# Optimization experiments

Measured on AMD Instinct MI355X. Metric: run time of the kernel, lower is better.

The kernel has to match this reference:

```python
import jax, jax.numpy as jnp
import numpy as np

DIM = 768
HEADS = 12
HD = DIM // HEADS  # 64
BASE = 100.0


def rope_sincos(H, W):
    # DINOv3 RopePositionEmbedding: normalize_coords='separate', base=100.0
    dd = HD // 4
    periods = BASE ** (jnp.arange(dd, dtype=jnp.float32) / dd)          # [dd]
    ch = (jnp.arange(H, dtype=jnp.float32) + 0.5) / H                    # pixel centers
    cw = (jnp.arange(W, dtype=jnp.float32) + 0.5) / W
    cy, cx = jnp.meshgrid(ch, cw, indexing='ij')
    coords = 2.0 * jnp.stack([cy, cx], axis=-1).reshape(H * W, 2) - 1.0  # [N,2] in [-1,1]
    angles = 2.0 * jnp.pi * coords[:, :, None] / periods[None, None, :]  # [N,2,dd]
    angles = angles.reshape(H * W, 2 * dd)                               # [N, HD//2]
    angles = jnp.concatenate([angles, angles], axis=-1)                  # [N, HD]
    return jnp.sin(angles), jnp.cos(angles)


def rotate_half(t):
    t1, t2 = jnp.split(t, 2, axis=-1)
    return jnp.concatenate([-t2, t1], axis=-1)


def setup_inputs() -> dict:
    key = jax.random.key(0)
    k1, k2, k3 = jax.random.split(key, 3)
    B, H, W = 2, 48, 48
    x = jax.random.normal(k1, (B, H, W, DIM), dtype=jnp.float32)
    w_qkv = jax.random.normal(k2, (3 * DIM, DIM), dtype=jnp.float32) * 0.02
    b_qkv = jnp.zeros((3 * DIM,), dtype=jnp.float32)
    w_proj = jax.random.normal(k3, (DIM, DIM), dtype=jnp.float32) * 0.02
    b_proj = jnp.zeros((DIM,), dtype=jnp.float32)
    return {"x": x, "w_qkv": w_qkv, "b_qkv": b_qkv, "w_proj": w_proj, "b_proj": b_proj}


def reference(x, w_qkv, b_qkv, w_proj, b_proj):
    B, H, W, C = x.shape
    N = H * W
    xf = x.reshape(B, N, C)
    qkv = xf @ w_qkv.T + b_qkv                                   # [B,N,3C]
    qkv = qkv.reshape(B, N, 3, HEADS, HD).transpose(2, 0, 3, 1, 4)
    q, k, v = qkv[0], qkv[1], qkv[2]                              # [B,h,N,d]
    sin, cos = rope_sincos(H, W)                                  # [N,d]
    q = q * cos + rotate_half(q) * sin
    k = k * cos + rotate_half(k) * sin
    scale = HD ** -0.5
    attn = jax.nn.softmax(jnp.einsum('bhqd,bhkd->bhqk', q, k) * scale, axis=-1)
    o = jnp.einsum('bhqk,bhkd->bhqd', attn, v)                    # [B,h,N,d]
    o = o.transpose(0, 2, 1, 3).reshape(B, N, C)
    o = o @ w_proj.T + b_proj
    return o.reshape(B, H, W, C)
```

## Files before the change

kernel.cpp:

```cpp
#include <hip/hip_runtime.h>

#define BATCH 2
#define NSEQ 2304
#define DIM 768
#define HEADS 12
#define HD 64
#define M_TOK (BATCH * NSEQ)
#define LDSP 72
#define KP 72
#define BH (BATCH * HEADS)
#define KT_HALF (NSEQ / 64 / 2)

typedef __attribute__((ext_vector_type(8))) short bf16x8;
typedef __attribute__((ext_vector_type(8))) short short8v;
typedef __attribute__((ext_vector_type(4))) float f32x4;
typedef __fp16 fp16x2 __attribute__((ext_vector_type(2)));
typedef _Float16 half4 __attribute__((ext_vector_type(4)));
typedef _Float16 half8 __attribute__((ext_vector_type(8)));

#define QSCALE (0.125f * 1.44269504088896f)
#define LOG2_100_D16 0.41524101186092029f

__device__ __forceinline__ short f2bf(float f) {
    union { float f; unsigned u; } v; v.f = f;
    unsigned r = v.u + 0x7fffu + ((v.u >> 16) & 1u);
    return (short)(r >> 16);
}

#define CN1 (M_TOK * DIM / 4)
#define CN2 (3 * DIM * DIM / 4)
#define CN3 (DIM * DIM / 4)
__global__ void cvt_all_kernel(const float* __restrict__ x, const float* __restrict__ wq,
                               const float* __restrict__ wp,
                               short* __restrict__ xb, short* __restrict__ wqb,
                               short* __restrict__ wpb) {
    int i = blockIdx.x * 256 + threadIdx.x;
    const float* src; short* dst; int j;
    if (i < CN1)              { src = x;  dst = xb;  j = i; }
    else if (i < CN1 + CN2)   { src = wq; dst = wqb; j = i - CN1; }
    else                      { src = wp; dst = wpb; j = i - CN1 - CN2; }
    float4 v = reinterpret_cast<const float4*>(src)[j];
    short4 o;
    o.x = f2bf(v.x); o.y = f2bf(v.y); o.z = f2bf(v.z); o.w = f2bf(v.w);
    reinterpret_cast<short4*>(dst)[j] = o;
}

__global__ __launch_bounds__(256) void gemm_qkv_kernel(
    const short* __restrict__ A,
    const short* __restrict__ Bt,
    const float* __restrict__ bias,
    short* __restrict__ qb, short* __restrict__ kbuf, _Float16* __restrict__ vtb)
{
    __shared__ __align__(16) short At[2][128 * LDSP];
    __shared__ __align__(16) short Bl[2][128 * LDSP];
    const int m0 = blockIdx.x * 128, n0 = blockIdx.y * 128;
    const int tid = threadIdx.x, lane = tid & 63, wave = tid >> 6;
    const int quad = lane >> 4, l16 = lane & 15;
    const int wm = (wave >> 1) * 64, wn = (wave & 1) * 64;
    const int r = tid >> 1, c0 = (tid & 1) * 32;
    f32x4 acc[4][4] = {};

    {
        const uint4* ga = reinterpret_cast<const uint4*>(&A[(size_t)(m0 + r) * DIM + c0]);
        const uint4* gb = reinterpret_cast<const uint4*>(&Bt[(size_t)(n0 + r) * DIM + c0]);
        uint4 a0 = ga[0], a1 = ga[1], a2 = ga[2], a3 = ga[3];
        uint4 b0 = gb[0], b1 = gb[1], b2 = gb[2], b3 = gb[3];
        uint4* sa = reinterpret_cast<uint4*>(&At[0][r * LDSP + c0]);
        uint4* sb = reinterpret_cast<uint4*>(&Bl[0][r * LDSP + c0]);
        sa[0] = a0; sa[1] = a1; sa[2] = a2; sa[3] = a3;
        sb[0] = b0; sb[1] = b1; sb[2] = b2; sb[3] = b3;
    }

    int cur = 0;
    for (int k0 = 0; k0 < DIM; k0 += 64) {
        __syncthreads();
        uint4 a0, a1, a2, a3, b0, b1, b2, b3;
        const bool pre = (k0 + 64 < DIM);
        if (pre) {
            const uint4* ga = reinterpret_cast<const uint4*>(&A[(size_t)(m0 + r) * DIM + k0 + 64 + c0]);
            const uint4* gb = reinterpret_cast<const uint4*>(&Bt[(size_t)(n0 + r) * DIM + k0 + 64 + c0]);
            a0 = ga[0]; a1 = ga[1]; a2 = ga[2]; a3 = ga[3];
            b0 = gb[0]; b1 = gb[1]; b2 = gb[2]; b3 = gb[3];
        }
#pragma unroll
        for (int ks = 0; ks < 2; ++ks) {
            bf16x8 af[4], bf[4];
#pragma unroll
            for (int mt = 0; mt < 4; ++mt)
                af[mt] = *reinterpret_cast<const bf16x8*>(&At[cur][(wm + mt * 16 + l16) * LDSP + ks * 32 + quad * 8]);
#pragma unroll
            for (int nt = 0; nt < 4; ++nt)
                bf[nt] = *reinterpret_cast<const bf16x8*>(&Bl[cur][(wn + nt * 16 + l16) * LDSP + ks * 32 + quad * 8]);
#pragma unroll
            for (int mt = 0; mt < 4; ++mt)
#pragma unroll
                for (int nt = 0; nt < 4; ++nt)
                    acc[mt][nt] = __builtin_amdgcn_mfma_f32_16x16x32_bf16(af[mt], bf[nt], acc[mt][nt], 0, 0, 0);
        }
        if (pre) {
            uint4* sa = reinterpret_cast<uint4*>(&At[cur ^ 1][r * LDSP + c0]);
            uint4* sb = reinterpret_cast<uint4*>(&Bl[cur ^ 1][r * LDSP + c0]);
            sa[0] = a0; sa[1] = a1; sa[2] = a2; sa[3] = a3;
            sb[0] = b0; sb[1] = b1; sb[2] = b2; sb[3] = b3;
        }
        cur ^= 1;
    }

    const int which = (n0 + wn) / DIM;
    const int head = ((n0 + wn) % DIM) / HD;
    const int b = m0 / NSEQ;
    const int tokb = m0 % NSEQ + wm;
    if (which == 2) {
#pragma unroll
        for (int mt = 0; mt < 4; ++mt)
#pragma unroll
            for (int nt = 0; nt < 4; ++nt) {
                const int n = n0 + wn + nt * 16 + l16;
                const int d = nt * 16 + l16;
                const float bi = bias[n];
                const int tok0 = tokb + mt * 16 + quad * 4;
                half4 hv;
                hv.x = (_Float16)(acc[mt][nt][0] + bi);
                hv.y = (_Float16)(acc[mt][nt][1] + bi);
                hv.z = (_Float16)(acc[mt][nt][2] + bi);
                hv.w = (_Float16)(acc[mt][nt][3] + bi);
                *reinterpret_cast<half4*>(&vtb[((size_t)(b * HEADS + head) * HD + d) * NSEQ + tok0]) = hv;
            }
    } else {
        short* dst = (which == 0) ? qb : kbuf;
        const float qs = (which == 0) ? QSCALE : 1.0f;
        float bi[4];
#pragma unroll
        for (int nt = 0; nt < 4; ++nt) bi[nt] = bias[n0 + wn + nt * 16 + l16];
        const float invp = __builtin_amdgcn_exp2f(-(float)l16 * LOG2_100_D16);
#pragma unroll
        for (int mt = 0; mt < 4; ++mt) {
#pragma unroll
            for (int rg = 0; rg < 4; ++rg) {
                const int tok = tokb + mt * 16 + quad * 4 + rg;
                const int yy = tok / 48, xx = tok - yy * 48;
                const float ry = (2.0f * (yy + 0.5f) * (1.0f / 48.0f) - 1.0f) * invp;
                const float rx = (2.0f * (xx + 0.5f) * (1.0f / 48.0f) - 1.0f) * invp;
                const float sy = __builtin_amdgcn_sinf(ry), cy = __builtin_amdgcn_cosf(ry);
                const float sx = __builtin_amdgcn_sinf(rx), cx = __builtin_amdgcn_cosf(rx);
                const float a0 = acc[mt][0][rg] + bi[0];
                const float a1 = acc[mt][1][rg] + bi[1];
                const float a2 = acc[mt][2][rg] + bi[2];
                const float a3 = acc[mt][3][rg] + bi[3];
                short* rp = &dst[((size_t)(b * HEADS + head) * NSEQ + tok) * HD];
                rp[l16]      = f2bf((a0 * cy - a2 * sy) * qs);
                rp[32 + l16] = f2bf((a2 * cy + a0 * sy) * qs);
                rp[16 + l16] = f2bf((a1 * cx - a3 * sx) * qs);
                rp[48 + l16] = f2bf((a3 * cx + a1 * sx) * qs);
            }
        }
    }
}

__global__ __launch_bounds__(256) void attn_kernel(
    const short* __restrict__ qb, const short* __restrict__ kb,
    const _Float16* __restrict__ vtb, _Float16* __restrict__ opart,
    float* __restrict__ lpart)
{
    __shared__ __align__(16) short    Kt[2][64 * KP];
    __shared__ __align__(16) _Float16 Vt[2][64 * KP];
    const int wg = blockIdx.x;
    const int xcd = wg & 7;
    const int slot = wg >> 3;
    const int slab = xcd * 6 + slot / 18;
    const int qt = slot % 18;
    const int kh = slab & 1;
    const int bh = slab >> 1;
    const int tid = threadIdx.x, lane = tid & 63, wave = tid >> 6;
    const int quad = lane >> 4, l16 = lane & 15;
    const int qrow0 = qt * 128 + wave * 32;
    const short* qbase = qb + (size_t)bh * NSEQ * HD;
    const short* kbase = kb + (size_t)bh * NSEQ * HD;
    const _Float16* vbase = vtb + (size_t)bh * HD * NSEQ;

    bf16x8 qf[2][2];
#pragma unroll
    for (int mt = 0; mt < 2; ++mt)
#pragma unroll
        for (int ks = 0; ks < 2; ++ks)
            qf[mt][ks] = *reinterpret_cast<const bf16x8*>(
                &qbase[(size_t)(qrow0 + mt * 16 + l16) * HD + ks * 32 + quad * 8]);

    half4 ones;
    ones.x = ones.y = ones.z = ones.w = (_Float16)1.0f;

    f32x4 oacc[2][4] = {};
    f32x4 lacc[2] = {};

    const int r = tid >> 2, cq = (tid & 3) * 16;
    const int t0 = kh * KT_HALF;
    const short* kp = kbase + (size_t)(t0 * 64 + r) * HD + cq;
    const _Float16* vp = vbase + (size_t)r * NSEQ + t0 * 64 + cq;
    {
        const uint4* gk = reinterpret_cast<const uint4*>(kp);
        uint4 k0 = gk[0], k1 = gk[1];
        const uint4* gv = reinterpret_cast<const uint4*>(vp);
        uint4 v0 = gv[0], v1 = gv[1];
        uint4* sk = reinterpret_cast<uint4*>(&Kt[0][r * KP + cq]);
        sk[0] = k0; sk[1] = k1;
        uint4* sv = reinterpret_cast<uint4*>(&Vt[0][r * KP + cq]);
        sv[0] = v0; sv[1] = v1;
        kp += 64 * HD;
        vp += 64;
    }

    int cur = 0;
    for (int kt = 0; kt < KT_HALF; ++kt) {
        __syncthreads();
        uint4 k0, k1, v0, v1;
        const bool pre = (kt + 1 < KT_HALF);
        if (pre) {
            const uint4* gk = reinterpret_cast<const uint4*>(kp);
            k0 = gk[0]; k1 = gk[1];
            const uint4* gv = reinterpret_cast<const uint4*>(vp);
            v0 = gv[0]; v1 = gv[1];
            kp += 64 * HD;
            vp += 64;
        }

        f32x4 sacc[4][2] = {};
#pragma unroll
        for (int ks = 0; ks < 2; ++ks) {
#pragma unroll
            for (int nt = 0; nt < 4; ++nt) {
                bf16x8 kf = *reinterpret_cast<const bf16x8*>(
                    &Kt[cur][(nt * 16 + l16) * KP + ks * 32 + quad * 8]);
#pragma unroll
                for (int mt = 0; mt < 2; ++mt)
                    sacc[nt][mt] = __builtin_amdgcn_mfma_f32_16x16x32_bf16(
                        kf, qf[mt][ks], sacc[nt][mt], 0, 0, 0);
            }
        }

        half4 pf[2][4];
#pragma unroll
        for (int mt = 0; mt < 2; ++mt)
#pragma unroll
            for (int nt = 0; nt < 4; ++nt) {
                fp16x2 lo = __builtin_amdgcn_cvt_pkrtz(
                    __builtin_amdgcn_exp2f(sacc[nt][mt][0]),
                    __builtin_amdgcn_exp2f(sacc[nt][mt][1]));
                fp16x2 hi = __builtin_amdgcn_cvt_pkrtz(
                    __builtin_amdgcn_exp2f(sacc[nt][mt][2]),
                    __builtin_amdgcn_exp2f(sacc[nt][mt][3]));
                half4 p;
                p.x = (_Float16)lo.x; p.y = (_Float16)lo.y;
                p.z = (_Float16)hi.x; p.w = (_Float16)hi.y;
                pf[mt][nt] = p;
            }

#pragma unroll
        for (int mt = 0; mt < 2; ++mt)
#pragma unroll
            for (int nt = 0; nt < 4; ++nt)
                lacc[mt] = __builtin_amdgcn_mfma_f32_16x16x16f16(
                    pf[mt][nt], ones, lacc[mt], 0, 0, 0);

#pragma unroll
        for (int nt = 0; nt < 4; ++nt)
#pragma unroll
            for (int dt = 0; dt < 4; ++dt) {
                half4 vf = *reinterpret_cast<const half4*>(
                    &Vt[cur][(dt * 16 + l16) * KP + nt * 16 + quad * 4]);
#pragma unroll
                for (int mt = 0; mt < 2; ++mt)
                    oacc[mt][dt] = __builtin_amdgcn_mfma_f32_16x16x16f16(
                        pf[mt][nt], vf, oacc[mt][dt], 0, 0, 0);
            }

        if (pre) {
            uint4* sk = reinterpret_cast<uint4*>(&Kt[cur ^ 1][r * KP + cq]);
            sk[0] = k0; sk[1] = k1;
            uint4* sv = reinterpret_cast<uint4*>(&Vt[cur ^ 1][r * KP + cq]);
            sv[0] = v0; sv[1] = v1;
        }
        cur ^= 1;
    }

    _Float16* ob2 = opart + (size_t)(kh * BH + bh) * NSEQ * HD;
    float* lp2 = lpart + (size_t)(kh * BH + bh) * NSEQ;
#pragma unroll
    for (int mt = 0; mt < 2; ++mt) {
#pragma unroll
        for (int dt = 0; dt < 4; ++dt)
#pragma unroll
            for (int rg = 0; rg < 4; ++rg) {
                int row = qrow0 + mt * 16 + quad * 4 + rg;
                ob2[(size_t)row * HD + dt * 16 + l16] = (_Float16)oacc[mt][dt][rg];
            }
        if (l16 == 0) {
#pragma unroll
            for (int rg = 0; rg < 4; ++rg)
                lp2[qrow0 + mt * 16 + quad * 4 + rg] = lacc[mt][rg];
        }
    }
}

__global__ __launch_bounds__(256) void gemm_proj_kernel(
    const _Float16* __restrict__ op,
    const float* __restrict__ lp,
    const short* __restrict__ Bt,
    const float* __restrict__ bias,
    float* __restrict__ out)
{
    __shared__ __align__(16) short At[64 * LDSP];
    __shared__ __align__(16) short Bl[64 * LDSP];
    const int m0 = blockIdx.x * 64, n0 = blockIdx.y * 64;
    const int tid = threadIdx.x, lane = tid & 63, wave = tid >> 6;
    const int quad = lane >> 4, l16 = lane & 15;
    const int wm = (wave >> 1) * 32, wn = (wave & 1) * 32;
    const int r = tid >> 2, cs = (tid & 3) * 16;
    const int b = m0 / NSEQ;
    const int tok = m0 % NSEQ + r;
    f32x4 acc[2][2] = {};

    for (int k0 = 0; k0 < DIM; k0 += 64) {
        const int h = k0 >> 6;
        const size_t pb = (size_t)(b * HEADS + h) * NSEQ + tok;
        const float l0 = lp[pb], l1 = lp[(size_t)BH * NSEQ + pb];
        const float inv = __builtin_amdgcn_rcpf(l0 + l1);
        const half8* o0 = reinterpret_cast<const half8*>(&op[pb * HD + cs]);
        const half8* o1 = reinterpret_cast<const half8*>(&op[(size_t)BH * NSEQ * HD + pb * HD + cs]);
        half8 p0 = o0[0], p1 = o0[1], q0 = o1[0], q1 = o1[1];
        const uint4* gb = reinterpret_cast<const uint4*>(&Bt[(size_t)(n0 + r) * DIM + k0 + cs]);
        uint4 bw0 = gb[0], bw1 = gb[1];
        short8v s0, s1;
#pragma unroll
        for (int j = 0; j < 8; ++j) {
            s0[j] = f2bf(((float)p0[j] + (float)q0[j]) * inv);
            s1[j] = f2bf(((float)p1[j] + (float)q1[j]) * inv);
        }
        *reinterpret_cast<short8v*>(&At[r * LDSP + cs]) = s0;
        *reinterpret_cast<short8v*>(&At[r * LDSP + cs + 8]) = s1;
        uint4* sb = reinterpret_cast<uint4*>(&Bl[r * LDSP + cs]);
        sb[0] = bw0; sb[1] = bw1;
        __syncthreads();
#pragma unroll
        for (int ks = 0; ks < 2; ++ks) {
            bf16x8 af[2], bf[2];
#pragma unroll
            for (int mt = 0; mt < 2; ++mt)
                af[mt] = *reinterpret_cast<const bf16x8*>(&At[(wm + mt * 16 + l16) * LDSP + ks * 32 + quad * 8]);
#pragma unroll
            for (int nt = 0; nt < 2; ++nt)
                bf[nt] = *reinterpret_cast<const bf16x8*>(&Bl[(wn + nt * 16 + l16) * LDSP + ks * 32 + quad * 8]);
#pragma unroll
            for (int mt = 0; mt < 2; ++mt)
#pragma unroll
                for (int nt = 0; nt < 2; ++nt)
                    acc[mt][nt] = __builtin_amdgcn_mfma_f32_16x16x32_bf16(af[mt], bf[nt], acc[mt][nt], 0, 0, 0);
        }
        __syncthreads();
    }

#pragma unroll
    for (int mt = 0; mt < 2; ++mt)
#pragma unroll
        for (int nt = 0; nt < 2; ++nt) {
            const int n = n0 + wn + nt * 16 + l16;
            const float bi = bias[n];
#pragma unroll
            for (int rg = 0; rg < 4; ++rg) {
                const int m = m0 + wm + mt * 16 + quad * 4 + rg;
                out[(size_t)m * DIM + n] = acc[mt][nt][rg] + bi;
            }
        }
}

extern "C" void kernel_launch(void* const* d_in, const int* in_sizes, int n_in,
                              void* d_out, int out_size, void* d_ws, size_t ws_size,
                              hipStream_t stream) {
    const float* x      = (const float*)d_in[0];
    const float* w_qkv  = (const float*)d_in[1];
    const float* b_qkv  = (const float*)d_in[2];
    const float* w_proj = (const float*)d_in[3];
    const float* b_proj = (const float*)d_in[4];
    float* out = (float*)d_out;

    short* xb     = (short*)d_ws;
    short* wqkvb  = xb + (size_t)M_TOK * DIM;
    short* wprojb = wqkvb + (size_t)3 * DIM * DIM;
    short* qb     = wprojb + (size_t)DIM * DIM;
    short* kb     = qb + (size_t)BH * NSEQ * HD;
    short* vtb    = kb + (size_t)BH * NSEQ * HD;
    short* opart  = vtb + (size_t)BH * NSEQ * HD;
    float* lpart  = (float*)(opart + (size_t)2 * BH * NSEQ * HD);

    cvt_all_kernel<<<(CN1 + CN2 + CN3) / 256, 256, 0, stream>>>(
        x, w_qkv, w_proj, xb, wqkvb, wprojb);

    dim3 g1(M_TOK / 128, 3 * DIM / 128);
    gemm_qkv_kernel<<<g1, 256, 0, stream>>>(xb, wqkvb, b_qkv, qb, kb, (_Float16*)vtb);

    attn_kernel<<<dim3(18 * 2 * BH), 256, 0, stream>>>(qb, kb, (const _Float16*)vtb,
                                                       (_Float16*)opart, lpart);

    dim3 g3(M_TOK / 64, DIM / 64);
    gemm_proj_kernel<<<g3, 256, 0, stream>>>((const _Float16*)opart, lpart,
                                             wprojb, b_proj, out);
}
```

Before: 190.6 us.

## Double attention query tile per wave to 64 rows and reuse K/V fragments

Each wave now handles 64 query rows instead of 32, so a workgroup covers 256 queries and the grid is halved. K and V fragments are loaded from LDS once per key tile into registers and reused across four query sub-tiles, cutting LDS reads and global K/V streaming per query. The cost is a larger register footprint (more accumulators and fragments), and launch_bounds(256,2) is added to constrain occupancy. With only 432 workgroups, fewer waves are in flight to hide latency.

```diff
diff --git a/kernel.cpp b/kernel.cpp
--- a/kernel.cpp
+++ b/kernel.cpp
@@ -157,7 +157,7 @@
     }
 }
 
-__global__ __launch_bounds__(256) void attn_kernel(
+__global__ __launch_bounds__(256, 2) void attn_kernel(
     const short* __restrict__ qb, const short* __restrict__ kb,
     const _Float16* __restrict__ vtb, _Float16* __restrict__ opart,
     float* __restrict__ lpart)
@@ -167,20 +167,20 @@
     const int wg = blockIdx.x;
     const int xcd = wg & 7;
     const int slot = wg >> 3;
-    const int slab = xcd * 6 + slot / 18;
-    const int qt = slot % 18;
+    const int slab = xcd * 6 + slot / 9;
+    const int qt = slot % 9;
     const int kh = slab & 1;
     const int bh = slab >> 1;
     const int tid = threadIdx.x, lane = tid & 63, wave = tid >> 6;
     const int quad = lane >> 4, l16 = lane & 15;
-    const int qrow0 = qt * 128 + wave * 32;
+    const int qrow0 = qt * 256 + wave * 64;
     const short* qbase = qb + (size_t)bh * NSEQ * HD;
     const short* kbase = kb + (size_t)bh * NSEQ * HD;
     const _Float16* vbase = vtb + (size_t)bh * HD * NSEQ;
 
-    bf16x8 qf[2][2];
-#pragma unroll
-    for (int mt = 0; mt < 2; ++mt)
+    bf16x8 qf[4][2];
+#pragma unroll
+    for (int mt = 0; mt < 4; ++mt)
 #pragma unroll
         for (int ks = 0; ks < 2; ++ks)
             qf[mt][ks] = *reinterpret_cast<const bf16x8*>(
@@ -189,8 +189,8 @@
     half4 ones;
     ones.x = ones.y = ones.z = ones.w = (_Float16)1.0f;
 
-    f32x4 oacc[2][4] = {};
-    f32x4 lacc[2] = {};
+    f32x4 oacc[4][4] = {};
+    f32x4 lacc[4] = {};
 
     const int r = tid >> 2, cq = (tid & 3) * 16;
     const int t0 = kh * KT_HALF;
@@ -223,55 +223,57 @@
             vp += 64;
         }
 
-        f32x4 sacc[4][2] = {};
-#pragma unroll
-        for (int ks = 0; ks < 2; ++ks) {
-#pragma unroll
-            for (int nt = 0; nt < 4; ++nt) {
-                bf16x8 kf = *reinterpret_cast<const bf16x8*>(
+        bf16x8 kf[2][4];
+#pragma unroll
+        for (int ks = 0; ks < 2; ++ks)
+#pragma unroll
+            for (int nt = 0; nt < 4; ++nt)
+                kf[ks][nt] = *reinterpret_cast<const bf16x8*>(
                     &Kt[cur][(nt * 16 + l16) * KP + ks * 32 + quad * 8]);
-#pragma unroll
-                for (int mt = 0; mt < 2; ++mt)
-                    sacc[nt][mt] = __builtin_amdgcn_mfma_f32_16x16x32_bf16(
-                        kf, qf[mt][ks], sacc[nt][mt], 0, 0, 0);
-            }
-        }
-
-        half4 pf[2][4];
-#pragma unroll
-        for (int mt = 0; mt < 2; ++mt)
+        half4 vf[4][4];
+#pragma unroll
+        for (int nt = 0; nt < 4; ++nt)
+#pragma unroll
+            for (int dt = 0; dt < 4; ++dt)
+                vf[nt][dt] = *reinterpret_cast<const half4*>(
+                    &Vt[cur][(dt * 16 + l16) * KP + nt * 16 + quad * 4]);
+
+#pragma unroll
+        for (int mt = 0; mt < 4; ++mt) {
+            f32x4 sacc[4] = {};
+#pragma unroll
+            for (int ks = 0; ks < 2; ++ks)
+#pragma unroll
+                for (int nt = 0; nt < 4; ++nt)
+                    sacc[nt] = __builtin_amdgcn_mfma_f32_16x16x32_bf16(
+                        kf[ks][nt], qf[mt][ks], sacc[nt], 0, 0, 0);
+
+            half4 pf[4];
 #pragma unroll
             for (int nt = 0; nt < 4; ++nt) {
                 fp16x2 lo = __builtin_amdgcn_cvt_pkrtz(
-                    __builtin_amdgcn_exp2f(sacc[nt][mt][0]),
-                    __builtin_amdgcn_exp2f(sacc[nt][mt][1]));
+                    __builtin_amdgcn_exp2f(sacc[nt][0]),
+                    __builtin_amdgcn_exp2f(sacc[nt][1]));
                 fp16x2 hi = __builtin_amdgcn_cvt_pkrtz(
-                    __builtin_amdgcn_exp2f(sacc[nt][mt][2]),
-                    __builtin_amdgcn_exp2f(sacc[nt][mt][3]));
+                    __builtin_amdgcn_exp2f(sacc[nt][2]),
+                    __builtin_amdgcn_exp2f(sacc[nt][3]));
                 half4 p;
                 p.x = (_Float16)lo.x; p.y = (_Float16)lo.y;
                 p.z = (_Float16)hi.x; p.w = (_Float16)hi.y;
-                pf[mt][nt] = p;
+                pf[nt] = p;
             }
 
-#pragma unroll
-        for (int mt = 0; mt < 2; ++mt)
 #pragma unroll
             for (int nt = 0; nt < 4; ++nt)
                 lacc[mt] = __builtin_amdgcn_mfma_f32_16x16x16f16(
-                    pf[mt][nt], ones, lacc[mt], 0, 0, 0);
-
-#pragma unroll
-        for (int nt = 0; nt < 4; ++nt)
-#pragma unroll
-            for (int dt = 0; dt < 4; ++dt) {
-                half4 vf = *reinterpret_cast<const half4*>(
-                    &Vt[cur][(dt * 16 + l16) * KP + nt * 16 + quad * 4]);
-#pragma unroll
-                for (int mt = 0; mt < 2; ++mt)
+                    pf[nt], ones, lacc[mt], 0, 0, 0);
+#pragma unroll
+            for (int nt = 0; nt < 4; ++nt)
+#pragma unroll
+                for (int dt = 0; dt < 4; ++dt)
                     oacc[mt][dt] = __builtin_amdgcn_mfma_f32_16x16x16f16(
-                        pf[mt][nt], vf, oacc[mt][dt], 0, 0, 0);
-            }
+                        pf[nt], vf[nt][dt], oacc[mt][dt], 0, 0, 0);
+        }
 
         if (pre) {
             uint4* sk = reinterpret_cast<uint4*>(&Kt[cur ^ 1][r * KP + cq]);
@@ -285,7 +287,7 @@
     _Float16* ob2 = opart + (size_t)(kh * BH + bh) * NSEQ * HD;
     float* lp2 = lpart + (size_t)(kh * BH + bh) * NSEQ;
 #pragma unroll
-    for (int mt = 0; mt < 2; ++mt) {
+    for (int mt = 0; mt < 4; ++mt) {
 #pragma unroll
         for (int dt = 0; dt < 4; ++dt)
 #pragma unroll
@@ -397,8 +399,8 @@
     dim3 g1(M_TOK / 128, 3 * DIM / 128);
     gemm_qkv_kernel<<<g1, 256, 0, stream>>>(xb, wqkvb, b_qkv, qb, kb, (_Float16*)vtb);
 
-    attn_kernel<<<dim3(18 * 2 * BH), 256, 0, stream>>>(qb, kb, (const _Float16*)vtb,
-                                                       (_Float16*)opart, lpart);
+    attn_kernel<<<dim3(9 * 2 * BH), 256, 0, stream>>>(qb, kb, (const _Float16*)vtb,
+                                                      (_Float16*)opart, lpart);
 
     dim3 g3(M_TOK / 64, DIM / 64);
     gemm_proj_kernel<<<g3, 256, 0, stream>>>((const _Float16*)opart, lpart,
```

Measured after the change: 173.4 us. 1.1x faster.
